# Kernel optimization log

Hardware: AMD Instinct MI355X
Metric: run time of the kernel (lower is better)

The kernel has to match this reference:

```python
import jax, jax.numpy as jnp
import numpy as np

N_NODES = 50000
N_EDGES = 800000
HID = 64
N_LAYERS = 3
N_GRAPHS = 64
NEG_SLOPE = 0.01  # nn.LeakyReLU default


def setup_inputs() -> dict:
    key = jax.random.key(0)
    ks = jax.random.split(key, 10)
    return {
        "x": jax.random.normal(ks[0], (N_NODES, HID), dtype=jnp.float32),
        "edge_attr": jax.random.normal(ks[1], (N_EDGES,), dtype=jnp.float32),
        "edge_w": jax.random.normal(ks[2], (N_LAYERS, 1, HID), dtype=jnp.float32) * 0.1,
        "edge_b": jax.random.normal(ks[3], (N_LAYERS, HID), dtype=jnp.float32) * 0.1,
        "node_w": jax.random.normal(ks[4], (N_LAYERS, 2 * HID, HID), dtype=jnp.float32) * 0.05,
        "node_b": jax.random.normal(ks[5], (N_LAYERS, HID), dtype=jnp.float32) * 0.1,
        "fc_w": jax.random.normal(ks[6], (HID, 1), dtype=jnp.float32) * 0.1,
        "fc_b": jax.random.normal(ks[7], (1,), dtype=jnp.float32) * 0.1,
        "edge_index": jax.random.randint(ks[8], (2, N_EDGES), 0, N_NODES, dtype=jnp.int32),
        "batch": jnp.sort(jax.random.randint(ks[9], (N_NODES,), 0, N_GRAPHS, dtype=jnp.int32)),
    }


def reference(x, edge_attr, edge_w, edge_b, node_w, node_b, fc_w, fc_b, edge_index, batch):
    src = edge_index[0]  # x_j gathered from source nodes
    dst = edge_index[1]  # aggregated into target nodes (aggr='add')
    ea = edge_attr.reshape(-1, 1)  # [E, 1]
    for l in range(N_LAYERS):
        edge_emb = ea @ edge_w[l] + edge_b[l]                       # [E, H] edge MLP
        msg = jnp.concatenate([x[src], edge_emb], axis=1)            # [E, 2H] message
        aggr = jax.ops.segment_sum(msg, dst, num_segments=N_NODES)   # [N, 2H] scatter-add
        x = jax.nn.relu(aggr @ node_w[l] + node_b[l])                # update: node MLP + ReLU
        x = jnp.where(x >= 0, x, NEG_SLOPE * x)                      # LeakyReLU (dropout=0)
    # global_mean_pool over batch assignment
    sums = jax.ops.segment_sum(x, batch, num_segments=N_GRAPHS)      # [G, H]
    counts = jax.ops.segment_sum(jnp.ones((x.shape[0], 1), x.dtype), batch, num_segments=N_GRAPHS)
    pooled = sums / jnp.maximum(counts, 1.0)
    return pooled @ fc_w + fc_b  # [G, 1]
```

## Files before the change

kernel.cpp:

```cpp
#include <hip/hip_runtime.h>

#define N_NODES 50000
#define N_EDGES 800000
#define HID 64
#define N_LAYERS 3
#define N_GRAPHS 64
#define MAXDEG 64
#define FIXS 4096.0f

typedef unsigned int u32;
typedef unsigned short ushort_t;
typedef short bf16x8 __attribute__((ext_vector_type(8)));
typedef float f32x4 __attribute__((ext_vector_type(4)));

__device__ __forceinline__ ushort_t f2bf(float f) {
    unsigned int u = __builtin_bit_cast(unsigned int, f);
    unsigned int r = u + 0x7fffu + ((u >> 16) & 1u);
    return (ushort_t)(r >> 16);
}
__device__ __forceinline__ float lo16(u32 u) { return __builtin_bit_cast(float, u << 16); }
__device__ __forceinline__ float hi16(u32 u) { return __builtin_bit_cast(float, u & 0xffff0000u); }

__global__ __launch_bounds__(256) void edge_cvt_uv_kernel(
        const int* __restrict__ src, const int* __restrict__ dst,
        const float* __restrict__ ea,
        int* __restrict__ cnt, u32* __restrict__ ell,
        const float* __restrict__ x_in, uint4* __restrict__ xbf0,
        const int* __restrict__ batch, int* __restrict__ gstart,
        const float* __restrict__ edge_w, const float* __restrict__ edge_b,
        const float* __restrict__ node_w, float* __restrict__ uv,
        int edgeBlocks, int cvtBlocks, int gbBlocks) {
    int t = threadIdx.x;
    int b = (int)blockIdx.x;
    if (b < edgeBlocks) {
        int e = b * 256 + t;
        if (e >= N_EDGES) return;
        int d = dst[e];
        float fv = (ea[e] + 8.0f) * FIXS;
        fv = fminf(fmaxf(fv, 0.0f), 65535.0f);
        u32 fx = __float2uint_rn(fv);
        int pos = atomicAdd(&cnt[d], 1);
        if (pos < MAXDEG) ell[((size_t)d << 6) + pos] = (u32)src[e] | (fx << 16);
        return;
    }
    if (b < edgeBlocks + cvtBlocks) {
        int i = (b - edgeBlocks) * 256 + t;
        if (i < N_NODES * HID / 8) {
            const float4* p = (const float4*)(x_in + (size_t)i * 8);
            float4 a = p[0], c = p[1];
            uint4 o;
            o.x = (u32)f2bf(a.x) | ((u32)f2bf(a.y) << 16);
            o.y = (u32)f2bf(a.z) | ((u32)f2bf(a.w) << 16);
            o.z = (u32)f2bf(c.x) | ((u32)f2bf(c.y) << 16);
            o.w = (u32)f2bf(c.z) | ((u32)f2bf(c.w) << 16);
            xbf0[i] = o;
        }
        return;
    }
    if (b < edgeBlocks + cvtBlocks + gbBlocks) {
        int i = (b - edgeBlocks - cvtBlocks) * 256 + t;
        if (i >= N_NODES) return;
        int bi = batch[i];
        if (i == 0) {
            for (int g = 0; g <= bi; g++) gstart[g] = 0;
        } else {
            int bp = batch[i - 1];
            for (int g = bp + 1; g <= bi; g++) gstart[g] = i;
        }
        if (i == N_NODES - 1) {
            for (int g = bi + 1; g <= N_GRAPHS; g++) gstart[g] = N_NODES;
        }
        return;
    }
    if (t >= N_LAYERS * HID) return;
    int l = t >> 6, hp = t & 63;
    const float* w2 = node_w + l * 2 * HID * HID + HID * HID + hp;
    float u = 0.f, v = 0.f;
    for (int h = 0; h < HID; h++) {
        float w = w2[h * HID];
        u += edge_w[l * HID + h] * w;
        v += edge_b[l * HID + h] * w;
    }
    uv[l * 2 * HID + hp]       = u;
    uv[l * 2 * HID + HID + hp] = v;
}

__global__ __launch_bounds__(128) void agg_mfma_kernel(
        const ushort_t* __restrict__ xbf, const u32* __restrict__ ell,
        const int* __restrict__ cnt,
        const float* __restrict__ W1, const float* __restrict__ node_b_l,
        const float* __restrict__ uv_l, float* __restrict__ sattr,
        int layer0, ushort_t* __restrict__ out_bf, float* __restrict__ out_f32) {
    __shared__ float redA[64][8];
    __shared__ float redB[64][8];
    __shared__ u32   redS[64];
    int lane = threadIdx.x & 63;
    int half = threadIdx.x >> 6;
    int nodeBase = blockIdx.x * 16;
    int q = lane >> 4, n15 = lane & 15;

    int m = nodeBase + n15;
    int dg = cnt[m]; if (dg > MAXDEG) dg = MAXDEG;
    int mx = dg;
#pragma unroll
    for (int off = 1; off < 16; off <<= 1) {
        int o = __shfl_xor(mx, off);
        mx = o > mx ? o : mx;
    }

    const uint4* erow4 = (const uint4*)(ell + ((size_t)m << 6));
    const uint4* xrows = (const uint4*)xbf;
    float accA[8] = {0,0,0,0,0,0,0,0};
    float accB[8] = {0,0,0,0,0,0,0,0};
    u32 sfix = 0;
    for (int base = half * 4; base < mx; base += 8) {
        uint4 e4 = erow4[base >> 2];
        u32 ee[4] = {e4.x, e4.y, e4.z, e4.w};
#pragma unroll
        for (int k = 0; k < 4; k++) {
            bool v = (base + k) < dg;
            u32 e = ee[k];
            sfix += v ? (e >> 16) : 0u;
            int s = v ? (int)(e & 0xffffu) : 0;
            uint4 lo = xrows[(size_t)s * 8 + q];
            uint4 hi = xrows[(size_t)s * 8 + 4 + q];
            float f = v ? 1.0f : 0.0f;
            accA[0] += f * lo16(lo.x); accA[1] += f * hi16(lo.x);
            accA[2] += f * lo16(lo.y); accA[3] += f * hi16(lo.y);
            accA[4] += f * lo16(lo.z); accA[5] += f * hi16(lo.z);
            accA[6] += f * lo16(lo.w); accA[7] += f * hi16(lo.w);
            accB[0] += f * lo16(hi.x); accB[1] += f * hi16(hi.x);
            accB[2] += f * lo16(hi.y); accB[3] += f * hi16(hi.y);
            accB[4] += f * lo16(hi.z); accB[5] += f * hi16(hi.z);
            accB[6] += f * lo16(hi.w); accB[7] += f * hi16(hi.w);
        }
    }

    if (half == 1) {
#pragma unroll
        for (int j = 0; j < 8; j++) { redA[lane][j] = accA[j]; redB[lane][j] = accB[j]; }
        redS[lane] = sfix;
    }
    __syncthreads();
    if (half == 1) return;
#pragma unroll
    for (int j = 0; j < 8; j++) { accA[j] += redA[lane][j]; accB[j] += redB[lane][j]; }
    sfix += redS[lane];

    float satv;
    if (layer0) {
        satv = (float)(int)sfix * (1.0f / FIXS) - 8.0f * (float)dg;
        if (lane < 16) sattr[nodeBase + lane] = satv;
    } else {
        satv = sattr[m];
    }

    bf16x8 af0, af1;
#pragma unroll
    for (int j = 0; j < 8; j++) {
        af0[j] = (short)f2bf(accA[j]);
        af1[j] = (short)f2bf(accB[j]);
    }

    int q8 = q * 8;
    f32x4 c[4];
#pragma unroll
    for (int nt = 0; nt < 4; nt++) {
        bf16x8 b0, b1;
#pragma unroll
        for (int j = 0; j < 8; j++) {
            b0[j] = (short)f2bf(W1[(q8 + j) * HID + nt * 16 + n15]);
            b1[j] = (short)f2bf(W1[(32 + q8 + j) * HID + nt * 16 + n15]);
        }
        f32x4 z = {0.f, 0.f, 0.f, 0.f};
        c[nt] = __builtin_amdgcn_mfma_f32_16x16x32_bf16(af0, b0, z, 0, 0, 0);
        c[nt] = __builtin_amdgcn_mfma_f32_16x16x32_bf16(af1, b1, c[nt], 0, 0, 0);
    }

    float dgown = (float)dg;
    float sat[4], dgf[4];
#pragma unroll
    for (int r = 0; r < 4; r++) {
        int srcLane = q * 4 + r;
        sat[r] = __shfl(satv, srcLane);
        dgf[r] = __shfl(dgown, srcLane);
    }
#pragma unroll
    for (int nt = 0; nt < 4; nt++) {
        int col = nt * 16 + n15;
        float uc = uv_l[col], vc = uv_l[HID + col], bc = node_b_l[col];
#pragma unroll
        for (int r = 0; r < 4; r++) {
            int n = nodeBase + q * 4 + r;
            float val = c[nt][r] + sat[r] * uc + dgf[r] * vc + bc;
            val = val > 0.f ? val : 0.f;
            if (out_bf) out_bf[(size_t)n * HID + col] = f2bf(val);
            else        out_f32[(size_t)n * HID + col] = val;
        }
    }
}

__global__ __launch_bounds__(256) void pool_fc_kernel(
        const float* __restrict__ x, const int* __restrict__ gstart,
        const float* __restrict__ fc_w, const float* __restrict__ fc_b,
        float* __restrict__ out) {
    __shared__ float red[4][HID];
    int g = blockIdx.x;
    int lane = threadIdx.x & 63, w = threadIdx.x >> 6;
    int s = gstart[g], e = gstart[g + 1];
    float acc = 0.f;
    int r = s + w;
    for (; r + 12 < e; r += 16) {
        float a0 = x[(size_t)(r     ) * HID + lane];
        float a1 = x[(size_t)(r +  4) * HID + lane];
        float a2 = x[(size_t)(r +  8) * HID + lane];
        float a3 = x[(size_t)(r + 12) * HID + lane];
        acc += a0 + a1 + a2 + a3;
    }
    for (; r < e; r += 4) acc += x[(size_t)r * HID + lane];
    red[w][lane] = acc;
    __syncthreads();
    if (w != 0) return;
    acc = red[0][lane] + red[1][lane] + red[2][lane] + red[3][lane];
    float dot = acc * fc_w[lane];
    for (int off = 32; off > 0; off >>= 1) dot += __shfl_down(dot, off);
    if (lane == 0) {
        float cntf = (float)(e - s);
        if (cntf < 1.f) cntf = 1.f;
        out[g] = dot / cntf + fc_b[0];
    }
}

extern "C" void kernel_launch(void* const* d_in, const int* in_sizes, int n_in,
                              void* d_out, int out_size, void* d_ws, size_t ws_size,
                              hipStream_t stream) {
    const float* x_in      = (const float*)d_in[0];
    const float* edge_attr = (const float*)d_in[1];
    const float* edge_w    = (const float*)d_in[2];
    const float* edge_b    = (const float*)d_in[3];
    const float* node_w    = (const float*)d_in[4];
    const float* node_b    = (const float*)d_in[5];
    const float* fc_w      = (const float*)d_in[6];
    const float* fc_b      = (const float*)d_in[7];
    const int*   edge_index= (const int*)d_in[8];
    const int*   batch     = (const int*)d_in[9];
    float* out = (float*)d_out;

    ushort_t* xbf0  = (ushort_t*)d_ws;
    ushort_t* xbf1  = xbf0 + (size_t)N_NODES * HID;
    float*    xA    = (float*)(xbf1 + (size_t)N_NODES * HID);
    u32*      ell   = (u32*)(xA + (size_t)N_NODES * HID);
    int*      cnt   = (int*)(ell + (size_t)N_NODES * MAXDEG);
    int*      gstart= cnt + N_NODES;
    float*    sattr = (float*)(gstart + N_GRAPHS + 1);
    float*    uv    = sattr + N_NODES;

    const int* src = edge_index;
    const int* dst = edge_index + N_EDGES;

    hipMemsetAsync(cnt, 0, (size_t)N_NODES * sizeof(int), stream);

    const int EB  = (N_EDGES + 255) / 256;
    const int CVT = (N_NODES * HID / 8 + 255) / 256;
    const int GB  = (N_NODES + 255) / 256;
    edge_cvt_uv_kernel<<<EB + CVT + GB + 1, 256, 0, stream>>>(
        src, dst, edge_attr, cnt, ell, x_in, (uint4*)xbf0, batch, gstart,
        edge_w, edge_b, node_w, uv, EB, CVT, GB);

    const int AGG_BLOCKS = N_NODES / 16;
    agg_mfma_kernel<<<AGG_BLOCKS, 128, 0, stream>>>(
        xbf0, ell, cnt, node_w, node_b, uv, sattr, 1, xbf1, nullptr);
    agg_mfma_kernel<<<AGG_BLOCKS, 128, 0, stream>>>(
        xbf1, ell, cnt, node_w + (size_t)2 * HID * HID, node_b + HID, uv + 2 * HID,
        sattr, 0, xbf0, nullptr);
    agg_mfma_kernel<<<AGG_BLOCKS, 128, 0, stream>>>(
        xbf0, ell, cnt, node_w + (size_t)4 * HID * HID, node_b + 2 * HID, uv + 4 * HID,
        sattr, 0, nullptr, xA);

    pool_fc_kernel<<<N_GRAPHS, 256, 0, stream>>>(xA, gstart, fc_w, fc_b, out);
}
```

Measured before the change: 214.3 us.

## Fuse mean-pool/FC into last aggregation layer and widen gather to four waves

The aggregation kernel now uses 256 threads per block, so four waves split each node's edge list, with partial sums reduced through shared memory. The separate pool+FC kernel is removed. In the last layer the final 64 blocks to finish, ordered by an atomic completion counter, spin until every block is done and then each pools one graph. This saves one launch and gives the gather more parallelism per node. The cost is spin-waiting blocks, a dependence on those blocks being resident, and idle waves during the MFMA phase.

```diff
diff --git a/kernel.cpp b/kernel.cpp
--- a/kernel.cpp
+++ b/kernel.cpp
@@ -7,6 +7,8 @@
 #define N_GRAPHS 64
 #define MAXDEG 64
 #define FIXS 4096.0f
+#define AGG_NBLK (N_NODES / 16)
+#define POOL_TAIL N_GRAPHS
 
 typedef unsigned int u32;
 typedef unsigned short ushort_t;
@@ -85,17 +87,21 @@
     uv[l * 2 * HID + HID + hp] = v;
 }
 
-__global__ __launch_bounds__(128) void agg_mfma_kernel(
+__global__ __launch_bounds__(256) void agg_mfma_kernel(
         const ushort_t* __restrict__ xbf, const u32* __restrict__ ell,
         const int* __restrict__ cnt,
         const float* __restrict__ W1, const float* __restrict__ node_b_l,
         const float* __restrict__ uv_l, float* __restrict__ sattr,
-        int layer0, ushort_t* __restrict__ out_bf, float* __restrict__ out_f32) {
-    __shared__ float redA[64][8];
-    __shared__ float redB[64][8];
-    __shared__ u32   redS[64];
+        int layer0, ushort_t* __restrict__ out_bf, float* __restrict__ out_f32,
+        int* __restrict__ done, const int* __restrict__ gstart,
+        const float* __restrict__ fc_w, const float* __restrict__ fc_b,
+        float* __restrict__ out) {
+    __shared__ float redA[3][64][8];
+    __shared__ float redB[3][64][8];
+    __shared__ u32   redS[3][64];
+    __shared__ int   sOld;
     int lane = threadIdx.x & 63;
-    int half = threadIdx.x >> 6;
+    int wv   = threadIdx.x >> 6;
     int nodeBase = blockIdx.x * 16;
     int q = lane >> 4, n15 = lane & 15;
 
@@ -113,7 +119,7 @@
     float accA[8] = {0,0,0,0,0,0,0,0};
     float accB[8] = {0,0,0,0,0,0,0,0};
     u32 sfix = 0;
-    for (int base = half * 4; base < mx; base += 8) {
+    for (int base = wv * 4; base < mx; base += 16) {
         uint4 e4 = erow4[base >> 2];
         u32 ee[4] = {e4.x, e4.y, e4.z, e4.w};
 #pragma unroll
@@ -136,92 +142,101 @@
         }
     }
 
-    if (half == 1) {
-#pragma unroll
-        for (int j = 0; j < 8; j++) { redA[lane][j] = accA[j]; redB[lane][j] = accB[j]; }
-        redS[lane] = sfix;
-    }
-    __syncthreads();
-    if (half == 1) return;
-#pragma unroll
-    for (int j = 0; j < 8; j++) { accA[j] += redA[lane][j]; accB[j] += redB[lane][j]; }
-    sfix += redS[lane];
-
-    float satv;
-    if (layer0) {
-        satv = (float)(int)sfix * (1.0f / FIXS) - 8.0f * (float)dg;
-        if (lane < 16) sattr[nodeBase + lane] = satv;
-    } else {
-        satv = sattr[m];
-    }
-
-    bf16x8 af0, af1;
-#pragma unroll
-    for (int j = 0; j < 8; j++) {
-        af0[j] = (short)f2bf(accA[j]);
-        af1[j] = (short)f2bf(accB[j]);
-    }
-
-    int q8 = q * 8;
-    f32x4 c[4];
-#pragma unroll
-    for (int nt = 0; nt < 4; nt++) {
-        bf16x8 b0, b1;
-#pragma unroll
-        for (int j = 0; j < 8; j++) {
-            b0[j] = (short)f2bf(W1[(q8 + j) * HID + nt * 16 + n15]);
-            b1[j] = (short)f2bf(W1[(32 + q8 + j) * HID + nt * 16 + n15]);
-        }
-        f32x4 z = {0.f, 0.f, 0.f, 0.f};
-        c[nt] = __builtin_amdgcn_mfma_f32_16x16x32_bf16(af0, b0, z, 0, 0, 0);
-        c[nt] = __builtin_amdgcn_mfma_f32_16x16x32_bf16(af1, b1, c[nt], 0, 0, 0);
-    }
-
-    float dgown = (float)dg;
-    float sat[4], dgf[4];
-#pragma unroll
-    for (int r = 0; r < 4; r++) {
-        int srcLane = q * 4 + r;
-        sat[r] = __shfl(satv, srcLane);
-        dgf[r] = __shfl(dgown, srcLane);
-    }
-#pragma unroll
-    for (int nt = 0; nt < 4; nt++) {
-        int col = nt * 16 + n15;
-        float uc = uv_l[col], vc = uv_l[HID + col], bc = node_b_l[col];
+    if (wv > 0) {
+#pragma unroll
+        for (int j = 0; j < 8; j++) { redA[wv-1][lane][j] = accA[j]; redB[wv-1][lane][j] = accB[j]; }
+        redS[wv-1][lane] = sfix;
+    }
+    __syncthreads();
+
+    if (wv == 0) {
+#pragma unroll
+        for (int p = 0; p < 3; p++) {
+#pragma unroll
+            for (int j = 0; j < 8; j++) { accA[j] += redA[p][lane][j]; accB[j] += redB[p][lane][j]; }
+            sfix += redS[p][lane];
+        }
+
+        float satv;
+        if (layer0) {
+            satv = (float)(int)sfix * (1.0f / FIXS) - 8.0f * (float)dg;
+            if (lane < 16) sattr[nodeBase + lane] = satv;
+        } else {
+            satv = sattr[m];
+        }
+
+        bf16x8 af0, af1;
+#pragma unroll
+        for (int j = 0; j < 8; j++) { af0[j] = (short)f2bf(accA[j]); af1[j] = (short)f2bf(accB[j]); }
+
+        int q8 = q * 8;
+        f32x4 c[4];
+#pragma unroll
+        for (int nt = 0; nt < 4; nt++) {
+            bf16x8 b0, b1;
+#pragma unroll
+            for (int j = 0; j < 8; j++) {
+                b0[j] = (short)f2bf(W1[(q8 + j) * HID + nt * 16 + n15]);
+                b1[j] = (short)f2bf(W1[(32 + q8 + j) * HID + nt * 16 + n15]);
+            }
+            f32x4 z = {0.f, 0.f, 0.f, 0.f};
+            c[nt] = __builtin_amdgcn_mfma_f32_16x16x32_bf16(af0, b0, z, 0, 0, 0);
+            c[nt] = __builtin_amdgcn_mfma_f32_16x16x32_bf16(af1, b1, c[nt], 0, 0, 0);
+        }
+
+        float dgown = (float)dg;
+        float sat[4], dgf[4];
 #pragma unroll
         for (int r = 0; r < 4; r++) {
-            int n = nodeBase + q * 4 + r;
-            float val = c[nt][r] + sat[r] * uc + dgf[r] * vc + bc;
-            val = val > 0.f ? val : 0.f;
-            if (out_bf) out_bf[(size_t)n * HID + col] = f2bf(val);
-            else        out_f32[(size_t)n * HID + col] = val;
-        }
-    }
-}
-
-__global__ __launch_bounds__(256) void pool_fc_kernel(
-        const float* __restrict__ x, const int* __restrict__ gstart,
-        const float* __restrict__ fc_w, const float* __restrict__ fc_b,
-        float* __restrict__ out) {
-    __shared__ float red[4][HID];
-    int g = blockIdx.x;
-    int lane = threadIdx.x & 63, w = threadIdx.x >> 6;
+            int srcLane = q * 4 + r;
+            sat[r] = __shfl(satv, srcLane);
+            dgf[r] = __shfl(dgown, srcLane);
+        }
+#pragma unroll
+        for (int nt = 0; nt < 4; nt++) {
+            int col = nt * 16 + n15;
+            float uc = uv_l[col], vc = uv_l[HID + col], bc = node_b_l[col];
+#pragma unroll
+            for (int r = 0; r < 4; r++) {
+                int n = nodeBase + q * 4 + r;
+                float val = c[nt][r] + sat[r] * uc + dgf[r] * vc + bc;
+                val = val > 0.f ? val : 0.f;
+                if (out_bf) out_bf[(size_t)n * HID + col] = f2bf(val);
+                else        out_f32[(size_t)n * HID + col] = val;
+            }
+        }
+    }
+    if (!out_f32) return;
+
+    if (wv == 0 && lane == 0) {
+        __threadfence();
+        sOld = __hip_atomic_fetch_add(done, 1, __ATOMIC_ACQ_REL, __HIP_MEMORY_SCOPE_AGENT);
+    }
+    __syncthreads();
+    int old = sOld;
+    if (old < AGG_NBLK - POOL_TAIL) return;
+    if (threadIdx.x == 0) {
+        while (__hip_atomic_load(done, __ATOMIC_ACQUIRE, __HIP_MEMORY_SCOPE_AGENT) < AGG_NBLK) {}
+    }
+    __syncthreads();
+
+    int g = old - (AGG_NBLK - POOL_TAIL);
     int s = gstart[g], e = gstart[g + 1];
     float acc = 0.f;
-    int r = s + w;
+    int r = s + wv;
     for (; r + 12 < e; r += 16) {
-        float a0 = x[(size_t)(r     ) * HID + lane];
-        float a1 = x[(size_t)(r +  4) * HID + lane];
-        float a2 = x[(size_t)(r +  8) * HID + lane];
-        float a3 = x[(size_t)(r + 12) * HID + lane];
+        float a0 = out_f32[(size_t)(r     ) * HID + lane];
+        float a1 = out_f32[(size_t)(r +  4) * HID + lane];
+        float a2 = out_f32[(size_t)(r +  8) * HID + lane];
+        float a3 = out_f32[(size_t)(r + 12) * HID + lane];
         acc += a0 + a1 + a2 + a3;
     }
-    for (; r < e; r += 4) acc += x[(size_t)r * HID + lane];
-    red[w][lane] = acc;
-    __syncthreads();
-    if (w != 0) return;
-    acc = red[0][lane] + red[1][lane] + red[2][lane] + red[3][lane];
+    for (; r < e; r += 4) acc += out_f32[(size_t)r * HID + lane];
+    float* pr = &redA[0][0][0];
+    pr[wv * 64 + lane] = acc;
+    __syncthreads();
+    if (wv != 0) return;
+    acc = pr[lane] + pr[64 + lane] + pr[128 + lane] + pr[192 + lane];
     float dot = acc * fc_w[lane];
     for (int off = 32; off > 0; off >>= 1) dot += __shfl_down(dot, off);
     if (lane == 0) {
@@ -251,14 +266,15 @@
     float*    xA    = (float*)(xbf1 + (size_t)N_NODES * HID);
     u32*      ell   = (u32*)(xA + (size_t)N_NODES * HID);
     int*      cnt   = (int*)(ell + (size_t)N_NODES * MAXDEG);
-    int*      gstart= cnt + N_NODES;
+    int*      done  = cnt + N_NODES;
+    int*      gstart= done + 1;
     float*    sattr = (float*)(gstart + N_GRAPHS + 1);
     float*    uv    = sattr + N_NODES;
 
     const int* src = edge_index;
     const int* dst = edge_index + N_EDGES;
 
-    hipMemsetAsync(cnt, 0, (size_t)N_NODES * sizeof(int), stream);
+    hipMemsetAsync(cnt, 0, ((size_t)N_NODES + 1) * sizeof(int), stream);
 
     const int EB  = (N_EDGES + 255) / 256;
     const int CVT = (N_NODES * HID / 8 + 255) / 256;
@@ -267,15 +283,15 @@
         src, dst, edge_attr, cnt, ell, x_in, (uint4*)xbf0, batch, gstart,
         edge_w, edge_b, node_w, uv, EB, CVT, GB);
 
-    const int AGG_BLOCKS = N_NODES / 16;
-    agg_mfma_kernel<<<AGG_BLOCKS, 128, 0, stream>>>(
-        xbf0, ell, cnt, node_w, node_b, uv, sattr, 1, xbf1, nullptr);
-    agg_mfma_kernel<<<AGG_BLOCKS, 128, 0, stream>>>(
+    agg_mfma_kernel<<<AGG_NBLK, 256, 0, stream>>>(
+        xbf0, ell, cnt, node_w, node_b, uv, sattr, 1, xbf1, nullptr,
+        nullptr, nullptr, nullptr, nullptr, nullptr);
+    agg_mfma_kernel<<<AGG_NBLK, 256, 0, stream>>>(
         xbf1, ell, cnt, node_w + (size_t)2 * HID * HID, node_b + HID, uv + 2 * HID,
-        sattr, 0, xbf0, nullptr);
-    agg_mfma_kernel<<<AGG_BLOCKS, 128, 0, stream>>>(
+        sattr, 0, xbf0, nullptr,
+        nullptr, nullptr, nullptr, nullptr, nullptr);
+    agg_mfma_kernel<<<AGG_NBLK, 256, 0, stream>>>(
         xbf0, ell, cnt, node_w + (size_t)4 * HID * HID, node_b + 2 * HID, uv + 4 * HID,
-        sattr, 0, nullptr, xA);
-
-    pool_fc_kernel<<<N_GRAPHS, 256, 0, stream>>>(xA, gstart, fc_w, fc_b, out);
-}
+        sattr, 0, nullptr, xA,
+        done, gstart, fc_w, fc_b, out);
+}
```

Result: slower. 420.9 us (+96.4%).
